# Kernel optimization log

Measured on AMD Instinct MI355X. Metric: run time of the kernel, lower is better.

Reference implementation:

```python
import jax, jax.numpy as jnp
import numpy as np

IMG = 32        # imgSize
NU = 96         # n_units per grid axis
SHAPE = IMG * NU
ALPHA = 0.9     # running_variance_alpha
EPS_LR = 1e-07


def setup_inputs() -> dict:
    key = jax.random.key(0)
    k1, k2 = jax.random.split(key)
    x = jax.random.uniform(k1, (IMG, IMG), dtype=jnp.float32)
    som = jnp.clip(0.1 + 0.3 * jax.random.normal(k2, (SHAPE, SHAPE), dtype=jnp.float32), 0.0, 1.0)
    running_variance = jnp.ones((SHAPE, SHAPE), jnp.float32)
    radius = 48.0 * jnp.ones((NU, NU), jnp.float32)
    learning_rates = 0.5 * jnp.ones((NU, NU), jnp.float32)
    bmu_count = jnp.zeros((NU, NU, 10), jnp.float32)
    return {"x": x, "som": som, "running_variance": running_variance,
            "radius": radius, "learning_rates": learning_rates, "bmu_count": bmu_count}


def reference(x, som, running_variance, radius, learning_rates, bmu_count):
    # --- layer1: variance-weighted squared distance of input to every unit tile ---
    som_b = som.reshape(NU, IMG, NU, IMG).transpose(0, 2, 1, 3)            # [NU,NU,IMG,IMG]
    var_b = running_variance.reshape(NU, IMG, NU, IMG).transpose(0, 2, 1, 3)
    diff = som_b - x                                                        # broadcast input over grid
    z = jnp.sum(diff * diff / var_b, axis=(2, 3))                           # [NU,NU] feature map
    # --- layer2: BMU = argmin over the unit grid ---
    flat = jnp.argmin(z)
    bi = flat // NU
    bj = flat % NU
    input_matrix = jnp.tile(x, (NU, NU))                                    # [SHAPE,SHAPE]
    # --- create_mask: neighborhood-weighted codebook + EMA variance update ---
    r = radius[bi, bj]
    lr_b = learning_rates[bi, bj]
    dm = 1.0 / (2.0 * r * r)                                                # distance_modifier
    constant = -jnp.log(EPS_LR / lr_b) / dm
    ii = jnp.arange(NU, dtype=jnp.float32)
    bif = bi.astype(jnp.float32)
    bjf = bj.astype(jnp.float32)
    cart = jnp.sqrt((ii[:, None] - bif) ** 2 + (ii[None, :] - bjf) ** 2)    # cartesian_distances[:,:,bi,bj]
    modifier = jnp.where(cart > r, 0.0, cart)
    fm = learning_rates * jnp.exp(-modifier) * dm                           # [NU,NU]
    fm_full = jnp.repeat(jnp.repeat(fm, IMG, axis=1), IMG, axis=0)          # [SHAPE,SHAPE]
    va = jnp.clip(ALPHA - 0.5 + jax.nn.sigmoid(cart / constant), 0.0, 1.0)
    va_full = jnp.repeat(jnp.repeat(va, IMG, axis=1), IMG, axis=0)
    new_som = som + fm_full * (input_matrix - som)
    new_var = va_full * running_variance + (1.0 - va_full) * (input_matrix - new_som) ** 2
    new_som = jnp.clip(new_som, 0.0, 1.0)
    # --- decayRadius / decayLearningRate at the BMU (per-class counts -> class 0 used) ---
    new_radius = jnp.maximum(radius.at[bi, bj].set(jnp.exp(-bmu_count[bi, bj, 0] / 15.0)), 1e-05)
    new_lr = jnp.maximum(learning_rates.at[bi, bj].set(jnp.exp(-bmu_count[bi, bj, 0] / 25.0)), 1e-05)
    return new_som, new_var, new_radius, new_lr
```

## Files before the change

### kernel.cpp

```cpp
#include <hip/hip_runtime.h>
#include <math.h>

#define NU 96
#define IMG 32
#define SHAPE (NU * IMG)
#define NUNITS (NU * NU)
#define PLANE (SHAPE * SHAPE)
#define SHAPE4 (SHAPE / 4)
#define IMG4 (IMG / 4)
#define NSLOTS 64

typedef float vfloat4 __attribute__((ext_vector_type(4)));


__global__ __launch_bounds__(256) void zargmin_kernel(const float* __restrict__ x,
                                                      const float* __restrict__ som,
                                                      const float* __restrict__ var,
                                                      unsigned long long* __restrict__ slots) {
    const int v = blockIdx.x, u = blockIdx.y, t = threadIdx.x;
    const int i = t >> 3, jv = t & 7;

    const vfloat4* __restrict__ som4 = (const vfloat4*)som;
    const vfloat4* __restrict__ var4 = (const vfloat4*)var;
    const vfloat4* __restrict__ x4   = (const vfloat4*)x;

    const int idx = (u * IMG + i) * SHAPE4 + v * IMG4 + jv;
    const vfloat4 s  = som4[idx];
    const vfloat4 w  = var4[idx];
    const vfloat4 xx = x4[i * IMG4 + jv];

    const vfloat4 d = s - xx;
    const vfloat4 q = d * d / w;
    float p = q.x + q.y + q.z + q.w;
    #pragma unroll
    for (int off = 32; off > 0; off >>= 1) p += __shfl_down(p, off, 64);

    __shared__ float lds[4];
    const int wave = t >> 6, lane = t & 63;
    if (lane == 0) lds[wave] = p;
    __syncthreads();
    if (t == 0) {
        const float z = lds[0] + lds[1] + lds[2] + lds[3];
        const unsigned int flat = (unsigned int)(u * NU + v);
        const unsigned long long key =
            ((unsigned long long)__float_as_uint(z) << 32) | (unsigned long long)flat;
        atomicMin(&slots[flat & (NSLOTS - 1)], key);
    }
}

__global__ __launch_bounds__(256) void update_kernel(const float* __restrict__ x,
                                                     const float* __restrict__ som,
                                                     const float* __restrict__ var,
                                                     const float* __restrict__ radius,
                                                     const float* __restrict__ lrates,
                                                     const float* __restrict__ bmu_count,
                                                     const unsigned long long* __restrict__ slots,
                                                     float* __restrict__ out) {
    const int v = blockIdx.x, u = blockIdx.y, t = threadIdx.x;

    unsigned long long key = slots[t & 63];
    #pragma unroll
    for (int off = 32; off > 0; off >>= 1) {
        const unsigned long long o = __shfl_xor(key, off, 64);
        key = (o < key) ? o : key;
    }
    const int flat = (int)(key & 0xFFFFFFFFull);
    const int bi = flat / NU, bj = flat - bi * NU;

    const float r    = radius[flat];
    const float lr_b = lrates[flat];
    const float dm   = 1.0f / (2.0f * r * r);
    const float constant = -logf(1e-7f / lr_b) / dm;

    const float du = (float)u - (float)bi;
    const float dv = (float)v - (float)bj;
    const float cart = sqrtf(du * du + dv * dv);
    const float modifier = (cart > r) ? 0.0f : cart;
    const float fm = lrates[u * NU + v] * expf(-modifier) * dm;
    const float sg = 1.0f / (1.0f + expf(-(cart / constant)));
    float va = 0.4f + sg;
    va = fminf(fmaxf(va, 0.0f), 1.0f);
    const float one_minus_va = 1.0f - va;

    const vfloat4* __restrict__ som4 = (const vfloat4*)som;
    const vfloat4* __restrict__ var4 = (const vfloat4*)var;
    const vfloat4* __restrict__ x4   = (const vfloat4*)x;
    vfloat4* __restrict__ out_som = (vfloat4*)out;
    vfloat4* __restrict__ out_var = (vfloat4*)(out + (size_t)PLANE);

    const int i = t >> 3, jv = t & 7;
    const int idx = (u * IMG + i) * SHAPE4 + v * IMG4 + jv;
    const vfloat4 s  = som4[idx];
    const vfloat4 w  = var4[idx];
    const vfloat4 xx = x4[i * IMG4 + jv];

    const vfloat4 n = s + fm * (xx - s);
    const vfloat4 d = xx - n;
    const vfloat4 nv = va * w + one_minus_va * d * d;
    vfloat4 ns;
    ns.x = fminf(fmaxf(n.x, 0.0f), 1.0f);
    ns.y = fminf(fmaxf(n.y, 0.0f), 1.0f);
    ns.z = fminf(fmaxf(n.z, 0.0f), 1.0f);
    ns.w = fminf(fmaxf(n.w, 0.0f), 1.0f);

    __builtin_nontemporal_store(ns, &out_som[idx]);
    __builtin_nontemporal_store(nv, &out_var[idx]);

    if (t == 0) {
        float* out_rad = out + 2 * (size_t)PLANE;
        float* out_lr  = out_rad + NUNITS;
        const int uv = u * NU + v;
        const float b0 = bmu_count[(size_t)flat * 10];
        const float rv = (uv == flat) ? expf(-b0 / 15.0f) : radius[uv];
        const float lv = (uv == flat) ? expf(-b0 / 25.0f) : lrates[uv];
        out_rad[uv] = fmaxf(rv, 1e-5f);
        out_lr[uv]  = fmaxf(lv, 1e-5f);
    }
}

extern "C" void kernel_launch(void* const* d_in, const int* in_sizes, int n_in,
                              void* d_out, int out_size, void* d_ws, size_t ws_size,
                              hipStream_t stream) {
    const float* x         = (const float*)d_in[0];
    const float* som       = (const float*)d_in[1];
    const float* var       = (const float*)d_in[2];
    const float* radius    = (const float*)d_in[3];
    const float* lrates    = (const float*)d_in[4];
    const float* bmu_count = (const float*)d_in[5];
    float* out = (float*)d_out;

    unsigned long long* slots = (unsigned long long*)d_ws;

    dim3 grid(NU, NU);
    zargmin_kernel<<<grid, 256, 0, stream>>>(x, som, var, slots);
    update_kernel<<<grid, 256, 0, stream>>>(x, som, var, radius, lrates, bmu_count, slots, out);
}
```

Before: 159.2 us.

## Assign one wave per unit tile in argmin and compute update scalars once per block

```diff
diff --git a/kernel.cpp b/kernel.cpp
--- a/kernel.cpp
+++ b/kernel.cpp
@@ -17,33 +17,34 @@
                                                       const float* __restrict__ som,
                                                       const float* __restrict__ var,
                                                       unsigned long long* __restrict__ slots) {
-    const int v = blockIdx.x, u = blockIdx.y, t = threadIdx.x;
-    const int i = t >> 3, jv = t & 7;
+    const int u = blockIdx.y;
+    const int wave = threadIdx.x >> 6, lane = threadIdx.x & 63;
+    const int v = blockIdx.x * 4 + wave;
+    const int i0 = lane >> 3, jv = lane & 7;
 
     const vfloat4* __restrict__ som4 = (const vfloat4*)som;
     const vfloat4* __restrict__ var4 = (const vfloat4*)var;
     const vfloat4* __restrict__ x4   = (const vfloat4*)x;
 
-    const int idx = (u * IMG + i) * SHAPE4 + v * IMG4 + jv;
-    const vfloat4 s  = som4[idx];
-    const vfloat4 w  = var4[idx];
-    const vfloat4 xx = x4[i * IMG4 + jv];
-
-    const vfloat4 d = s - xx;
-    const vfloat4 q = d * d / w;
-    float p = q.x + q.y + q.z + q.w;
+    float p = 0.0f;
+    #pragma unroll
+    for (int k = 0; k < 4; ++k) {
+        const int row = i0 + 8 * k;
+        const int idx = (u * IMG + row) * SHAPE4 + v * IMG4 + jv;
+        const vfloat4 s  = som4[idx];
+        const vfloat4 w  = var4[idx];
+        const vfloat4 xx = x4[row * IMG4 + jv];
+        const vfloat4 d = s - xx;
+        const vfloat4 q = d * d / w;
+        p += q.x + q.y + q.z + q.w;
+    }
     #pragma unroll
     for (int off = 32; off > 0; off >>= 1) p += __shfl_down(p, off, 64);
 
-    __shared__ float lds[4];
-    const int wave = t >> 6, lane = t & 63;
-    if (lane == 0) lds[wave] = p;
-    __syncthreads();
-    if (t == 0) {
-        const float z = lds[0] + lds[1] + lds[2] + lds[3];
+    if (lane == 0) {
         const unsigned int flat = (unsigned int)(u * NU + v);
         const unsigned long long key =
-            ((unsigned long long)__float_as_uint(z) << 32) | (unsigned long long)flat;
+            ((unsigned long long)__float_as_uint(p) << 32) | (unsigned long long)flat;
         atomicMin(&slots[flat & (NSLOTS - 1)], key);
     }
 }
@@ -58,28 +59,41 @@
                                                      float* __restrict__ out) {
     const int v = blockIdx.x, u = blockIdx.y, t = threadIdx.x;
 
-    unsigned long long key = slots[t & 63];
-    #pragma unroll
-    for (int off = 32; off > 0; off >>= 1) {
-        const unsigned long long o = __shfl_xor(key, off, 64);
-        key = (o < key) ? o : key;
+    __shared__ float sh_fm, sh_va;
+    __shared__ int   sh_flat;
+
+    if (t < 64) {
+        unsigned long long key = slots[t];
+        #pragma unroll
+        for (int off = 32; off > 0; off >>= 1) {
+            const unsigned long long o = __shfl_xor(key, off, 64);
+            key = (o < key) ? o : key;
+        }
+        if (t == 0) {
+            const int flat = (int)(key & 0xFFFFFFFFull);
+            const int bi = flat / NU, bj = flat - bi * NU;
+
+            const float r    = radius[flat];
+            const float lr_b = lrates[flat];
+            const float dm   = 1.0f / (2.0f * r * r);
+            const float constant = -logf(1e-7f / lr_b) / dm;
+
+            const float du = (float)u - (float)bi;
+            const float dv = (float)v - (float)bj;
+            const float cart = sqrtf(du * du + dv * dv);
+            const float modifier = (cart > r) ? 0.0f : cart;
+            const float fm = lrates[u * NU + v] * expf(-modifier) * dm;
+            const float sg = 1.0f / (1.0f + expf(-(cart / constant)));
+            float va = 0.4f + sg;
+            va = fminf(fmaxf(va, 0.0f), 1.0f);
+
+            sh_fm = fm; sh_va = va; sh_flat = flat;
+        }
     }
-    const int flat = (int)(key & 0xFFFFFFFFull);
-    const int bi = flat / NU, bj = flat - bi * NU;
+    __syncthreads();
 
-    const float r    = radius[flat];
-    const float lr_b = lrates[flat];
-    const float dm   = 1.0f / (2.0f * r * r);
-    const float constant = -logf(1e-7f / lr_b) / dm;
-
-    const float du = (float)u - (float)bi;
-    const float dv = (float)v - (float)bj;
-    const float cart = sqrtf(du * du + dv * dv);
-    const float modifier = (cart > r) ? 0.0f : cart;
-    const float fm = lrates[u * NU + v] * expf(-modifier) * dm;
-    const float sg = 1.0f / (1.0f + expf(-(cart / constant)));
-    float va = 0.4f + sg;
-    va = fminf(fmaxf(va, 0.0f), 1.0f);
+    const float fm = sh_fm;
+    const float va = sh_va;
     const float one_minus_va = 1.0f - va;
 
     const vfloat4* __restrict__ som4 = (const vfloat4*)som;
@@ -109,6 +123,7 @@
     if (t == 0) {
         float* out_rad = out + 2 * (size_t)PLANE;
         float* out_lr  = out_rad + NUNITS;
+        const int flat = sh_flat;
         const int uv = u * NU + v;
         const float b0 = bmu_count[(size_t)flat * 10];
         const float rv = (uv == flat) ? expf(-b0 / 15.0f) : radius[uv];
@@ -131,7 +146,8 @@
 
     unsigned long long* slots = (unsigned long long*)d_ws;
 
-    dim3 grid(NU, NU);
-    zargmin_kernel<<<grid, 256, 0, stream>>>(x, som, var, slots);
-    update_kernel<<<grid, 256, 0, stream>>>(x, som, var, radius, lrates, bmu_count, slots, out);
+    dim3 grid_z(NU / 4, NU);
+    dim3 grid_u(NU, NU);
+    zargmin_kernel<<<grid_z, 256, 0, stream>>>(x, som, var, slots);
+    update_kernel<<<grid_u, 256, 0, stream>>>(x, som, var, radius, lrates, bmu_count, slots, out);
 }
```

Result: slower. 167.4 us (+5.1%).
